# Kernel optimization log

Measured on AMD Instinct MI355X. Metric: run time of the kernel, lower is better.

## Reference

```python
import jax, jax.numpy as jnp
import numpy as np

A, N, B, S = 100, 256, 128, 1024  # alphabet, num_states, batch, max seq len


def setup_inputs() -> dict:
    key = jax.random.key(0)
    k1, k2, k3, k4, k5 = jax.random.split(key, 5)
    xs = jax.random.randint(k1, (B, S), 0, A)                     # symbols
    lengths = jax.random.randint(k2, (B,), 1, S + 1)              # lengths in [1, S]
    scale = np.float32(1.0 / np.sqrt(N))
    W = jax.random.normal(k3, (A, N, N), jnp.float32) * scale     # transition matrices
    lin_w = jax.random.normal(k4, (2, N), jnp.float32) * scale    # accept/reject head
    lin_b = jax.random.normal(k5, (2,), jnp.float32) * 0.01
    return {"xs": xs, "lengths": lengths, "W": W, "lin_w": lin_w, "lin_b": lin_b}


def reference(xs, lengths, W, lin_w, lin_b):
    Bsz = xs.shape[0]
    Nst = W.shape[1]
    # h0 = one-hot of state 0, matching F.one_hot(zeros)
    h0 = jnp.zeros((Bsz, Nst), W.dtype).at[:, 0].set(1.0)

    def step(h, x_t):
        # W[x_t]: [B, N, N]; h: [B, N] -> h_new = W[x_t] @ h
        h_new = jnp.einsum("bij,bj->bi", W[x_t], h)
        return h_new, h_new

    _, hs = jax.lax.scan(step, h0, xs.T)          # hs: [S, B, N]
    h_final = hs[lengths - 1, jnp.arange(Bsz)]    # state at position lengths-1, [B, N]
    return h_final @ lin_w.T + lin_b              # [B, 2]
```

## Files before the change

kernel.cpp:

```cpp
#include <hip/hip_runtime.h>
#include <hip/hip_fp16.h>

#define NSTATES 256
#define SEQ 1024
#define NSYM 100

__global__ __launch_bounds__(256) void prep_k(const float* __restrict__ W,
                                              __half* __restrict__ WT) {
    __shared__ float tile[32][33];
    int a = blockIdx.y;
    int t = blockIdx.x;
    int tr = (t >> 3) << 5;
    int tc = (t & 7) << 5;
    const float* src = W + (size_t)a * (NSTATES * NSTATES);
    __half* dst = WT + (size_t)a * (NSTATES * NSTATES);
    int x = threadIdx.x & 31;
    int y4 = threadIdx.x >> 5;
#pragma unroll
    for (int yy = 0; yy < 4; yy++) {
        int y = y4 * 4 + yy;
        tile[y][x] = src[(size_t)(tr + y) * NSTATES + tc + x];
    }
    __syncthreads();
#pragma unroll
    for (int yy = 0; yy < 4; yy++) {
        int y = y4 * 4 + yy;
        dst[(size_t)(tc + y) * NSTATES + tr + x] = __float2half(tile[x][y]);
    }
}

__global__ __launch_bounds__(1024) void pann_fwd_h(const int* __restrict__ xs,
                                                   const int* __restrict__ lengths,
                                                   const __half* __restrict__ WT,
                                                   const float* __restrict__ lin_w,
                                                   const float* __restrict__ lin_b,
                                                   float* __restrict__ out) {
    __shared__ float h[NSTATES];
    __shared__ float partial[16][NSTATES];
    __shared__ int xrow[SEQ];

    int b = blockIdx.x;
    int tid = threadIdx.x;
    int w = tid >> 6;
    int lane = tid & 63;

    xrow[tid] = xs[(size_t)b * SEQ + tid];
    if (tid < NSTATES) h[tid] = (tid == 0) ? 1.0f : 0.0f;
    int len = lengths[b];
    __syncthreads();

    int jbase = w << 4;
    const ushort4* W4 = (const ushort4*)WT;
    const ushort4* wl = W4 + jbase * 64 + lane;

    ushort4 Ra[16], Rb[16];
    {
        int x0 = __builtin_amdgcn_readfirstlane(xrow[0]);
        const ushort4* p = wl + (size_t)x0 * 16384;
#pragma unroll
        for (int jj = 0; jj < 16; jj++) Ra[jj] = p[jj * 64];
    }

    int t = 0;
#define PHASE(RCUR, RNXT)                                                     \
    {                                                                         \
        int tn = t + 1; if (tn >= len) tn = t;                                \
        int xn = __builtin_amdgcn_readfirstlane(xrow[tn]);                    \
        const ushort4* pn = wl + (size_t)xn * 16384;                          \
        _Pragma("unroll")                                                     \
        for (int jj = 0; jj < 16; jj++) RNXT[jj] = pn[jj * 64];               \
        float ax = 0.f, ay = 0.f, az = 0.f, aw = 0.f;                         \
        _Pragma("unroll")                                                     \
        for (int jj = 0; jj < 16; jj++) {                                     \
            float hj = h[jbase + jj];                                         \
            float2 f0 = __half22float2(*(const __half2*)&RCUR[jj].x);         \
            float2 f1 = __half22float2(*(const __half2*)&RCUR[jj].z);         \
            ax = fmaf(f0.x, hj, ax);                                          \
            ay = fmaf(f0.y, hj, ay);                                          \
            az = fmaf(f1.x, hj, az);                                          \
            aw = fmaf(f1.y, hj, aw);                                          \
        }                                                                     \
        *(float4*)&partial[w][lane << 2] = make_float4(ax, ay, az, aw);       \
        __syncthreads();                                                      \
        if (tid < NSTATES) {                                                  \
            float s = 0.f;                                                    \
            _Pragma("unroll")                                                 \
            for (int ww = 0; ww < 16; ww++) s += partial[ww][tid];            \
            h[tid] = s;                                                       \
        }                                                                     \
        __syncthreads();                                                      \
        t++;                                                                  \
    }

    while (t < len) {
        PHASE(Ra, Rb);
        if (t >= len) break;
        PHASE(Rb, Ra);
    }
#undef PHASE

    if (tid < NSTATES) {
        float hv = h[tid];
        partial[0][tid] = hv * lin_w[tid];
        partial[1][tid] = hv * lin_w[NSTATES + tid];
    }
    __syncthreads();
    for (int s = 128; s > 0; s >>= 1) {
        if (tid < s) {
            partial[0][tid] += partial[0][tid + s];
            partial[1][tid] += partial[1][tid + s];
        }
        __syncthreads();
    }
    if (tid == 0) {
        out[b * 2 + 0] = partial[0][0] + lin_b[0];
        out[b * 2 + 1] = partial[1][0] + lin_b[1];
    }
}

__global__ __launch_bounds__(1024) void pann_fwd_nt(const int* __restrict__ xs,
                                                    const int* __restrict__ lengths,
                                                    const float* __restrict__ W,
                                                    const float* __restrict__ lin_w,
                                                    const float* __restrict__ lin_b,
                                                    float* __restrict__ out) {
    __shared__ float hbuf[2][NSTATES];
    __shared__ float opart[2][NSTATES];
    __shared__ int xrow[SEQ];

    int b = blockIdx.x;
    int tid = threadIdx.x;
    int w = tid >> 6;
    int lane = tid & 63;

    xrow[tid] = xs[(size_t)b * SEQ + tid];
    if (tid < NSTATES) hbuf[0][tid] = (tid == 0) ? 1.0f : 0.0f;
    int len = lengths[b];
    __syncthreads();

    int cur = 0;
    for (int t = 0; t < len; t++) {
        int x = xrow[t];
        const float4* wp = (const float4*)(W + (size_t)x * (NSTATES * NSTATES));
        float4 hv = *(const float4*)&hbuf[cur][lane << 2];
#pragma unroll
        for (int ii = 0; ii < 4; ii++) {
            int i = (w << 4) + ii * 4;
#pragma unroll
            for (int k = 0; k < 4; k++) {
                int row = i + k;
                float4 wv = wp[row * 64 + lane];
                float p = wv.x * hv.x + wv.y * hv.y + wv.z * hv.z + wv.w * hv.w;
#pragma unroll
                for (int off = 32; off > 0; off >>= 1) p += __shfl_down(p, off);
                if (lane == 0) hbuf[cur ^ 1][row] = p;
            }
        }
        __syncthreads();
        cur ^= 1;
    }

    if (tid < NSTATES) {
        float hv = hbuf[cur][tid];
        opart[0][tid] = hv * lin_w[tid];
        opart[1][tid] = hv * lin_w[NSTATES + tid];
    }
    __syncthreads();
    for (int s = 128; s > 0; s >>= 1) {
        if (tid < s) {
            opart[0][tid] += opart[0][tid + s];
            opart[1][tid] += opart[1][tid + s];
        }
        __syncthreads();
    }
    if (tid == 0) {
        out[b * 2 + 0] = opart[0][0] + lin_b[0];
        out[b * 2 + 1] = opart[1][0] + lin_b[1];
    }
}

extern "C" void kernel_launch(void* const* d_in, const int* in_sizes, int n_in,
                              void* d_out, int out_size, void* d_ws, size_t ws_size,
                              hipStream_t stream) {
    const int* xs = (const int*)d_in[0];
    const int* lengths = (const int*)d_in[1];
    const float* W = (const float*)d_in[2];
    const float* lin_w = (const float*)d_in[3];
    const float* lin_b = (const float*)d_in[4];
    float* out = (float*)d_out;

    int B = in_sizes[0] / SEQ;
    size_t wbytes = (size_t)NSYM * NSTATES * NSTATES * sizeof(__half);

    if (ws_size >= wbytes) {
        __half* WT = (__half*)d_ws;
        dim3 tg(64, NSYM);
        prep_k<<<tg, 256, 0, stream>>>(W, WT);
        pann_fwd_h<<<B, 1024, 0, stream>>>(xs, lengths, WT, lin_w, lin_b, out);
    } else {
        pann_fwd_nt<<<B, 1024, 0, stream>>>(xs, lengths, W, lin_w, lin_b, out);
    }
}
```

Baseline: 2.147 ms.

## Re-block fp16 weights so each wave owns 16 output rows and reduces via shuffles

The fp16 weight copy is re-laid out so each wave holds a 16-row band of outputs across all 256 inputs instead of a 16-column slice. Each wave now reduces its partial sums with xor-shuffles and writes finished h entries directly into a double-buffered h array. This removes the shared-memory partial array, the cross-wave reduction pass and one of the two block barriers per step in the serial recurrence. The cost is extra shuffle instructions per step and h reads strided across lanes, which may cause LDS bank conflicts.

Result: slower. 2.203 ms (+2.6%).

```diff
diff --git a/kernel.cpp b/kernel.cpp
--- a/kernel.cpp
+++ b/kernel.cpp
@@ -5,38 +5,33 @@
 #define SEQ 1024
 #define NSYM 100
 
-__global__ __launch_bounds__(256) void prep_k(const float* __restrict__ W,
-                                              __half* __restrict__ WT) {
-    __shared__ float tile[32][33];
+__global__ __launch_bounds__(256) void prep_b(const float* __restrict__ W,
+                                              __half* __restrict__ WB) {
+    __shared__ float tile[16][256];
     int a = blockIdx.y;
-    int t = blockIdx.x;
-    int tr = (t >> 3) << 5;
-    int tc = (t & 7) << 5;
-    const float* src = W + (size_t)a * (NSTATES * NSTATES);
-    __half* dst = WT + (size_t)a * (NSTATES * NSTATES);
-    int x = threadIdx.x & 31;
-    int y4 = threadIdx.x >> 5;
-#pragma unroll
-    for (int yy = 0; yy < 4; yy++) {
-        int y = y4 * 4 + yy;
-        tile[y][x] = src[(size_t)(tr + y) * NSTATES + tc + x];
-    }
-    __syncthreads();
-#pragma unroll
-    for (int yy = 0; yy < 4; yy++) {
-        int y = y4 * 4 + yy;
-        dst[(size_t)(tc + y) * NSTATES + tr + x] = __float2half(tile[x][y]);
-    }
-}
-
-__global__ __launch_bounds__(1024) void pann_fwd_h(const int* __restrict__ xs,
+    int w = blockIdx.x;
+    int t = threadIdx.x;
+    const float* src = W + ((size_t)a * 256 + w * 16) * 256;
+#pragma unroll
+    for (int r = 0; r < 16; r++) tile[r][t] = src[r * 256 + t];
+    __syncthreads();
+    __half tmp[16];
+#pragma unroll
+    for (int i = 0; i < 16; i++) tmp[i] = __float2half(tile[i][t]);
+    ushort4* dst = (ushort4*)(WB + ((((size_t)a * 16 + w) * 256) + t) * 16);
+    const ushort4* s = (const ushort4*)tmp;
+#pragma unroll
+    for (int q = 0; q < 4; q++) dst[q] = s[q];
+}
+
+__global__ __launch_bounds__(1024) void pann_fwd_b(const int* __restrict__ xs,
                                                    const int* __restrict__ lengths,
-                                                   const __half* __restrict__ WT,
+                                                   const __half* __restrict__ WB,
                                                    const float* __restrict__ lin_w,
                                                    const float* __restrict__ lin_b,
                                                    float* __restrict__ out) {
-    __shared__ float h[NSTATES];
-    __shared__ float partial[16][NSTATES];
+    __shared__ float h[2][NSTATES];
+    __shared__ float opart[2][NSTATES];
     __shared__ int xrow[SEQ];
 
     int b = blockIdx.x;
@@ -45,50 +40,54 @@
     int lane = tid & 63;
 
     xrow[tid] = xs[(size_t)b * SEQ + tid];
-    if (tid < NSTATES) h[tid] = (tid == 0) ? 1.0f : 0.0f;
+    if (tid < NSTATES) h[0][tid] = (tid == 0) ? 1.0f : 0.0f;
     int len = lengths[b];
     __syncthreads();
 
-    int jbase = w << 4;
-    const ushort4* W4 = (const ushort4*)WT;
-    const ushort4* wl = W4 + jbase * 64 + lane;
+    const ushort4* Wb4 = (const ushort4*)WB;
+    const ushort4* wl = Wb4 + w * 1024 + lane;
+    int hidx = lane >> 2;
 
     ushort4 Ra[16], Rb[16];
     {
         int x0 = __builtin_amdgcn_readfirstlane(xrow[0]);
         const ushort4* p = wl + (size_t)x0 * 16384;
 #pragma unroll
-        for (int jj = 0; jj < 16; jj++) Ra[jj] = p[jj * 64];
-    }
-
+        for (int k = 0; k < 16; k++) Ra[k] = p[k * 64];
+    }
+
+    int cur = 0;
     int t = 0;
-#define PHASE(RCUR, RNXT)                                                     \
+#define PHASE(RC, RN)                                                         \
     {                                                                         \
         int tn = t + 1; if (tn >= len) tn = t;                                \
         int xn = __builtin_amdgcn_readfirstlane(xrow[tn]);                    \
         const ushort4* pn = wl + (size_t)xn * 16384;                          \
         _Pragma("unroll")                                                     \
-        for (int jj = 0; jj < 16; jj++) RNXT[jj] = pn[jj * 64];               \
-        float ax = 0.f, ay = 0.f, az = 0.f, aw = 0.f;                         \
+        for (int k = 0; k < 16; k++) RN[k] = pn[k * 64];                      \
+        float a0 = 0.f, a1 = 0.f, a2 = 0.f, a3 = 0.f;                         \
         _Pragma("unroll")                                                     \
-        for (int jj = 0; jj < 16; jj++) {                                     \
-            float hj = h[jbase + jj];                                         \
-            float2 f0 = __half22float2(*(const __half2*)&RCUR[jj].x);         \
-            float2 f1 = __half22float2(*(const __half2*)&RCUR[jj].z);         \
-            ax = fmaf(f0.x, hj, ax);                                          \
-            ay = fmaf(f0.y, hj, ay);                                          \
-            az = fmaf(f1.x, hj, az);                                          \
-            aw = fmaf(f1.y, hj, aw);                                          \
+        for (int k = 0; k < 16; k++) {                                        \
+            float hj = h[cur][k * 16 + hidx];                                 \
+            float2 f0 = __half22float2(*(const __half2*)&RC[k].x);            \
+            float2 f1 = __half22float2(*(const __half2*)&RC[k].z);            \
+            a0 = fmaf(f0.x, hj, a0);                                          \
+            a1 = fmaf(f0.y, hj, a1);                                          \
+            a2 = fmaf(f1.x, hj, a2);                                          \
+            a3 = fmaf(f1.y, hj, a3);                                          \
         }                                                                     \
-        *(float4*)&partial[w][lane << 2] = make_float4(ax, ay, az, aw);       \
+        _Pragma("unroll")                                                     \
+        for (int m = 4; m <= 32; m <<= 1) {                                   \
+            a0 += __shfl_xor(a0, m, 64);                                      \
+            a1 += __shfl_xor(a1, m, 64);                                      \
+            a2 += __shfl_xor(a2, m, 64);                                      \
+            a3 += __shfl_xor(a3, m, 64);                                      \
+        }                                                                     \
+        if (lane < 4)                                                         \
+            *(float4*)&h[cur ^ 1][w * 16 + lane * 4] =                        \
+                make_float4(a0, a1, a2, a3);                                  \
         __syncthreads();                                                      \
-        if (tid < NSTATES) {                                                  \
-            float s = 0.f;                                                    \
-            _Pragma("unroll")                                                 \
-            for (int ww = 0; ww < 16; ww++) s += partial[ww][tid];            \
-            h[tid] = s;                                                       \
-        }                                                                     \
-        __syncthreads();                                                      \
+        cur ^= 1;                                                             \
         t++;                                                                  \
     }
 
@@ -100,21 +99,21 @@
 #undef PHASE
 
     if (tid < NSTATES) {
-        float hv = h[tid];
-        partial[0][tid] = hv * lin_w[tid];
-        partial[1][tid] = hv * lin_w[NSTATES + tid];
+        float hv = h[cur][tid];
+        opart[0][tid] = hv * lin_w[tid];
+        opart[1][tid] = hv * lin_w[NSTATES + tid];
     }
     __syncthreads();
     for (int s = 128; s > 0; s >>= 1) {
         if (tid < s) {
-            partial[0][tid] += partial[0][tid + s];
-            partial[1][tid] += partial[1][tid + s];
+            opart[0][tid] += opart[0][tid + s];
+            opart[1][tid] += opart[1][tid + s];
         }
         __syncthreads();
     }
     if (tid == 0) {
-        out[b * 2 + 0] = partial[0][0] + lin_b[0];
-        out[b * 2 + 1] = partial[1][0] + lin_b[1];
+        out[b * 2 + 0] = opart[0][0] + lin_b[0];
+        out[b * 2 + 1] = opart[1][0] + lin_b[1];
     }
 }
 
@@ -193,10 +192,10 @@
     size_t wbytes = (size_t)NSYM * NSTATES * NSTATES * sizeof(__half);
 
     if (ws_size >= wbytes) {
-        __half* WT = (__half*)d_ws;
-        dim3 tg(64, NSYM);
-        prep_k<<<tg, 256, 0, stream>>>(W, WT);
-        pann_fwd_h<<<B, 1024, 0, stream>>>(xs, lengths, WT, lin_w, lin_b, out);
+        __half* WB = (__half*)d_ws;
+        dim3 tg(16, NSYM);
+        prep_b<<<tg, 256, 0, stream>>>(W, WB);
+        pann_fwd_b<<<B, 1024, 0, stream>>>(xs, lengths, WB, lin_w, lin_b, out);
     } else {
         pann_fwd_nt<<<B, 1024, 0, stream>>>(xs, lengths, W, lin_w, lin_b, out);
     }
```
